# Performance work log

Measured on AMD Instinct MI355X. Metric: run time of the kernel, lower is better.

## Reference

```python
import jax, jax.numpy as jnp
import numpy as np

DECAY = 0.99
EPS = 1e-05
LOSS_FACTOR = 0.1


def setup_inputs() -> dict:
    key = jax.random.key(0)
    k1, k2, k3, k4 = jax.random.split(key, 4)
    x = jax.random.normal(k1, (64, 256, 32, 32), dtype=jnp.float32)
    centroids = jax.random.normal(k2, (256, 1024), dtype=jnp.float32)
    cluster_size = jax.random.uniform(k3, (1024,), dtype=jnp.float32)
    centroids_avg = jax.random.normal(k4, (256, 1024), dtype=jnp.float32)
    return {"x": x, "centroids": centroids, "cluster_size": cluster_size,
            "centroids_avg": centroids_avg}


def _forward(x, centroids, cluster_size, centroids_avg):
    F, K = centroids.shape
    # torch: x_flat = x.transpose(-1, 1).contiguous().view(-1, n_features)
    xs = jnp.swapaxes(x, 1, -1)              # [B, W, H, C]
    flat_shape = xs.shape
    xf = xs.reshape(-1, F)                   # [N, F]
    dist = ((xf * xf).sum(1, keepdims=True)
            + (centroids * centroids).sum(0, keepdims=True)
            - 2.0 * (xf @ centroids))        # [N, K]
    ind = jnp.argmin(dist, axis=1)           # [N] nearest centroid
    # training-path EMA updates (one-hot matmuls expressed as segment sums)
    counts = jax.ops.segment_sum(jnp.ones(ind.shape, dtype=xf.dtype), ind,
                                 num_segments=K)              # [K]
    centroids_sum = jax.ops.segment_sum(xf, ind, num_segments=K).T  # [F, K]
    new_cs = DECAY * cluster_size + (1.0 - DECAY) * counts
    new_avg = DECAY * centroids_avg + (1.0 - DECAY) * centroids_sum
    n = new_cs.sum()
    cs_norm = (new_cs + EPS) / (n + K * EPS) * n
    new_centroids = new_avg / cs_norm[None, :]               # [F, K]
    # quantize with updated codebook (embedding lookup)
    xq = new_centroids.T[ind].reshape(flat_shape)            # [B, W, H, C]
    xq = jnp.swapaxes(xq, 1, -1)                             # [B, C, H, W]
    xq_st = x + jax.lax.stop_gradient(xq - x)                # straight-through
    return xq_st, xq


def reference(x, centroids, cluster_size, centroids_avg):
    out, _ = _forward(x, centroids, cluster_size, centroids_avg)
    return out
```

## Files before the change

### kernel.cpp

```cpp
#include <hip/hip_runtime.h>


#define DECAY 0.99f
#define EPSF 1e-5f
#define DELTA 0.05f

typedef _Float16 f16x8 __attribute__((ext_vector_type(8)));
typedef float f32x4 __attribute__((ext_vector_type(4)));

static __device__ __forceinline__ unsigned short h_bits(_Float16 h) {
  return __builtin_bit_cast(unsigned short, h);
}
static __device__ __forceinline__ float h_val(unsigned short u) {
  return (float)__builtin_bit_cast(_Float16, u);
}

__global__ void centT_kernel(const float* __restrict__ cent, _Float16* __restrict__ ctp,
                             float* __restrict__ csq, unsigned int* __restrict__ counts,
                             unsigned int* __restrict__ flagcnt) {
  __shared__ float tl[32][33];
  const int bid = blockIdx.x;
  const int f0 = (bid >> 5) * 32, k0 = (bid & 31) * 32;
  const int t = threadIdx.x;
#pragma unroll
  for (int i = 0; i < 4; ++i) {
    int fi = (t >> 5) + i * 8, ki = t & 31;
    tl[fi][ki] = cent[(size_t)(f0 + fi) * 1024 + k0 + ki];
  }
  __syncthreads();
#pragma unroll
  for (int i = 0; i < 4; ++i) {
    int ki = (t >> 5) + i * 8, fi = t & 31;
    int k = k0 + ki, f = f0 + fi;
    _Float16 h = (_Float16)tl[fi][ki];
    size_t idx = (size_t)(k >> 4) * 4096 + (size_t)(f >> 5) * 512 +
                 (size_t)(k & 15) * 32 + (size_t)((f >> 3) & 3) * 8 + (f & 7);
    ctp[idx] = h;
  }
  if (bid < 32) {
    __shared__ float red[8][32];
    const int kk = k0 + (t & 31);
    const int fg = t >> 5;
    float s = 0.f;
    for (int f = fg * 32; f < fg * 32 + 32; ++f) {
      float v = cent[(size_t)f * 1024 + kk];
      s += v * v;
    }
    red[fg][t & 31] = s;
    __syncthreads();
    if (t < 32) {
      float tot = 0.f;
#pragma unroll
      for (int g = 0; g < 8; ++g) tot += red[g][t];
      csq[k0 + t] = tot;
    }
  }
  if (bid == 32) {
    counts[t] = 0u;
    counts[t + 256] = 0u;
    counts[t + 512] = 0u;
    counts[t + 768] = 0u;
    if (t == 0) *flagcnt = 0u;
  }
}

__global__ void transpose_kernel(const float* __restrict__ x, _Float16* __restrict__ xh) {
  __shared__ float tile[64][65];
  int bid = blockIdx.x;
  int pt = bid & 15, ct = (bid >> 4) & 3, b = bid >> 6;
  int c0 = ct * 64, p0 = pt * 64;
  int t = threadIdx.x;
#pragma unroll
  for (int i = 0; i < 4; ++i) {
    int idx = t + i * 256;
    int ci = idx >> 4, pq = idx & 15;
    float4 v = *(const float4*)&x[((size_t)(b * 256 + c0 + ci) << 10) + p0 + pq * 4];
    tile[ci][pq * 4 + 0] = v.x;
    tile[ci][pq * 4 + 1] = v.y;
    tile[ci][pq * 4 + 2] = v.z;
    tile[ci][pq * 4 + 3] = v.w;
  }
  __syncthreads();
#pragma unroll
  for (int i = 0; i < 2; ++i) {
    int idx = t + i * 256;
    int pi = idx >> 3, cg = idx & 7;
    int p = p0 + pi;
    int r = ((p & 31) << 5) | (p >> 5);
    unsigned int wd[4];
#pragma unroll
    for (int j = 0; j < 4; ++j) {
      float v0 = tile[cg * 8 + j * 2][pi];
      float v1 = tile[cg * 8 + j * 2 + 1][pi];
      wd[j] = (unsigned int)h_bits((_Float16)v0) |
              ((unsigned int)h_bits((_Float16)v1) << 16);
    }
    uint4 u = {wd[0], wd[1], wd[2], wd[3]};
    *(uint4*)((unsigned int*)xh + (size_t)((b << 10) + r) * 128 + ct * 32 + cg * 4) = u;
  }
}

__global__ __launch_bounds__(256, 2) void mfma_argmin_kernel(
    const _Float16* __restrict__ xh, const _Float16* __restrict__ ctp,
    const float* __restrict__ csq, int* __restrict__ ind,
    int* __restrict__ flaglist, unsigned int* __restrict__ flagcnt,
    unsigned int* __restrict__ counts) {
  __shared__ _Float16 Ah[64 * 256];
  __shared__ _Float16 Bst[4 * 2 * 4 * 512];
  __shared__ float csql[1024];
  __shared__ float red1[4][64], red2[4][64];
  __shared__ int redk[4][64];
  const int t = threadIdx.x;
  const int lane = t & 63, w = t >> 6;
  const int lr = lane & 15, lg = lane >> 4;
  const int n0 = blockIdx.x * 64;

#pragma unroll
  for (int i = 0; i < 4; ++i) csql[t + i * 256] = csq[t + i * 256];
#pragma unroll
  for (int i = 0; i < 8; ++i) {
    int idx = t + i * 256;
    int row = idx >> 5, c16 = (idx & 31) * 16;
    int sw = c16 ^ ((row & 7) << 4);
    *(f16x8*)((char*)Ah + row * 512 + sw) =
        *(const f16x8*)((const char*)xh + (size_t)(n0 + row) * 512 + c16);
  }
  __syncthreads();

  float b1[4][4], b2v[4][4];
  int bk[4][4];
#pragma unroll
  for (int rt = 0; rt < 4; ++rt)
#pragma unroll
    for (int rg = 0; rg < 4; ++rg) { b1[rt][rg] = 3.4e38f; b2v[rt][rg] = 3.4e38f; bk[rt][rg] = 0; }

  const int swz = (lr & 7) << 4;
  const int boffh = (lr * 4 + lg) * 8;
  const size_t lgo = (size_t)lane * 16;
  _Float16* bw = &Bst[w * 4096];

#define DMA4(CHB, KS, P)                                                              \
  do {                                                                                \
    const char* g_ = (const char*)ctp + (CHB) + (size_t)(KS) * 1024 + lgo;            \
    _Float16* l_ = bw + (P) * 2048;                                                   \
    __builtin_amdgcn_global_load_lds(                                                 \
        (const __attribute__((address_space(1))) unsigned int*)(g_),                  \
        (__attribute__((address_space(3))) unsigned int*)(l_), 16, 0, 0);             \
    __builtin_amdgcn_global_load_lds(                                                 \
        (const __attribute__((address_space(1))) unsigned int*)(g_ + 8192),           \
        (__attribute__((address_space(3))) unsigned int*)(l_ + 512), 16, 0, 0);       \
    __builtin_amdgcn_global_load_lds(                                                 \
        (const __attribute__((address_space(1))) unsigned int*)(g_ + 16384),          \
        (__attribute__((address_space(3))) unsigned int*)(l_ + 1024), 16, 0, 0);      \
    __builtin_amdgcn_global_load_lds(                                                 \
        (const __attribute__((address_space(1))) unsigned int*)(g_ + 24576),          \
        (__attribute__((address_space(3))) unsigned int*)(l_ + 1536), 16, 0, 0);      \
  } while (0)

#define KSHALF(KS, P, WN)                                                             \
  do {                                                                                \
    asm volatile("s_waitcnt vmcnt(" WN ")" ::: "memory");                             \
    __builtin_amdgcn_sched_barrier(0);                                                \
    const _Float16* bp_ = bw + (P) * 2048 + boffh;                                    \
    f16x8 q0 = *(const f16x8*)(bp_);                                                  \
    f16x8 q1 = *(const f16x8*)(bp_ + 512);                                            \
    f16x8 q2 = *(const f16x8*)(bp_ + 1024);                                           \
    f16x8 q3 = *(const f16x8*)(bp_ + 1536);                                           \
    const char* ap_ = (const char*)Ah + lr * 512 + (((KS) * 64 + lg * 16) ^ swz);     \
    f16x8 p0 = *(const f16x8*)(ap_);                                                  \
    f16x8 p1 = *(const f16x8*)(ap_ + 8192);                                           \
    f16x8 p2 = *(const f16x8*)(ap_ + 16384);                                          \
    f16x8 p3 = *(const f16x8*)(ap_ + 24576);                                          \
    acc[0][0] = __builtin_amdgcn_mfma_f32_16x16x32_f16(p0, q0, acc[0][0], 0, 0, 0);   \
    acc[0][1] = __builtin_amdgcn_mfma_f32_16x16x32_f16(p1, q0, acc[0][1], 0, 0, 0);   \
    acc[0][2] = __builtin_amdgcn_mfma_f32_16x16x32_f16(p2, q0, acc[0][2], 0, 0, 0);   \
    acc[0][3] = __builtin_amdgcn_mfma_f32_16x16x32_f16(p3, q0, acc[0][3], 0, 0, 0);   \
    acc[1][0] = __builtin_amdgcn_mfma_f32_16x16x32_f16(p0, q1, acc[1][0], 0, 0, 0);   \
    acc[1][1] = __builtin_amdgcn_mfma_f32_16x16x32_f16(p1, q1, acc[1][1], 0, 0, 0);   \
    acc[1][2] = __builtin_amdgcn_mfma_f32_16x16x32_f16(p2, q1, acc[1][2], 0, 0, 0);   \
    acc[1][3] = __builtin_amdgcn_mfma_f32_16x16x32_f16(p3, q1, acc[1][3], 0, 0, 0);   \
    acc[2][0] = __builtin_amdgcn_mfma_f32_16x16x32_f16(p0, q2, acc[2][0], 0, 0, 0);   \
    acc[2][1] = __builtin_amdgcn_mfma_f32_16x16x32_f16(p1, q2, acc[2][1], 0, 0, 0);   \
    acc[2][2] = __builtin_amdgcn_mfma_f32_16x16x32_f16(p2, q2, acc[2][2], 0, 0, 0);   \
    acc[2][3] = __builtin_amdgcn_mfma_f32_16x16x32_f16(p3, q2, acc[2][3], 0, 0, 0);   \
    acc[3][0] = __builtin_amdgcn_mfma_f32_16x16x32_f16(p0, q3, acc[3][0], 0, 0, 0);   \
    acc[3][1] = __builtin_amdgcn_mfma_f32_16x16x32_f16(p1, q3, acc[3][1], 0, 0, 0);   \
    acc[3][2] = __builtin_amdgcn_mfma_f32_16x16x32_f16(p2, q3, acc[3][2], 0, 0, 0);   \
    acc[3][3] = __builtin_amdgcn_mfma_f32_16x16x32_f16(p3, q3, acc[3][3], 0, 0, 0);   \
  } while (0)

  size_t chb = (size_t)w * 131072;
  DMA4(chb, 0, 0);
  DMA4(chb, 1, 1);
#pragma unroll 1
  for (int ch = 0; ch < 4; ++ch) {
    const int ccb = w * 256 + ch * 64;
    f32x4 acc[4][4];
#pragma unroll
    for (int ct = 0; ct < 4; ++ct)
#pragma unroll
      for (int rt = 0; rt < 4; ++rt) acc[ct][rt] = (f32x4){0.f, 0.f, 0.f, 0.f};

    KSHALF(0, 0, "4");  DMA4(chb, 2, 0);
    KSHALF(1, 1, "4");  DMA4(chb, 3, 1);
    KSHALF(2, 0, "4");  DMA4(chb, 4, 0);
    KSHALF(3, 1, "4");  DMA4(chb, 5, 1);
    KSHALF(4, 0, "4");  DMA4(chb, 6, 0);
    KSHALF(5, 1, "4");  DMA4(chb, 7, 1);
    KSHALF(6, 0, "4");
    if (ch < 3) {
      DMA4(chb + 32768, 0, 0);
      KSHALF(7, 1, "4");
      DMA4(chb + 32768, 1, 1);
    } else {
      KSHALF(7, 1, "0");
    }

#pragma unroll
    for (int ct = 0; ct < 4; ++ct) {
      const int col = ccb + ct * 16 + lr;
      const float cq = csql[col];
#pragma unroll
      for (int rt = 0; rt < 4; ++rt)
#pragma unroll
        for (int rg = 0; rg < 4; ++rg) {
          float d = cq - 2.f * acc[ct][rt][rg];
          if (d < b1[rt][rg]) {
            b2v[rt][rg] = b1[rt][rg];
            b1[rt][rg] = d;
            bk[rt][rg] = col;
          } else if (d < b2v[rt][rg]) {
            b2v[rt][rg] = d;
          }
        }
    }
    chb += 32768;
  }
#undef DMA4
#undef KSHALF

#pragma unroll
  for (int rt = 0; rt < 4; ++rt)
#pragma unroll
    for (int rg = 0; rg < 4; ++rg) {
      float v1 = b1[rt][rg], v2 = b2v[rt][rg];
      int kk = bk[rt][rg];
#pragma unroll
      for (int off = 8; off >= 1; off >>= 1) {
        float o1 = __shfl_xor(v1, off);
        int ok = __shfl_xor(kk, off);
        float o2 = __shfl_xor(v2, off);
        float nb2 = fminf(fmaxf(v1, o1), fminf(v2, o2));
        if (o1 < v1 || (o1 == v1 && ok < kk)) { v1 = o1; kk = ok; }
        v2 = nb2;
      }
      if (lr == 0) {
        int row = rt * 16 + lg * 4 + rg;
        red1[w][row] = v1;
        redk[w][row] = kk;
        red2[w][row] = v2;
      }
    }
  __syncthreads();
  if (t < 64) {
    float v1 = red1[0][t], v2 = red2[0][t];
    int kk = redk[0][t];
#pragma unroll
    for (int wi = 1; wi < 4; ++wi) {
      float o1 = red1[wi][t], o2 = red2[wi][t];
      int ok = redk[wi][t];
      float nb2 = fminf(fmaxf(v1, o1), fminf(v2, o2));
      if (o1 < v1 || (o1 == v1 && ok < kk)) { v1 = o1; kk = ok; }
      v2 = nb2;
    }
    ind[n0 + t] = kk;
    atomicAdd(&counts[kk], 1u);
    if (v2 - v1 < DELTA) {
      unsigned int p = atomicAdd(flagcnt, 1u);
      flaglist[p] = n0 + t;
    }
  }
}

__global__ __launch_bounds__(256) void fixup_kernel(
    const float* __restrict__ x, const float* __restrict__ cent,
    const float* __restrict__ csq, const int* __restrict__ flaglist,
    const unsigned int* __restrict__ flagcnt, int* __restrict__ ind,
    unsigned int* __restrict__ counts) {
  const int t = threadIdx.x;
  const int nf = (int)*flagcnt;
  __shared__ float xrow[4][256];
  __shared__ int rows[4];
  __shared__ float rv[256];
  __shared__ int rk[256];
  for (int base = blockIdx.x * 4; base < nf; base += gridDim.x * 4) {
    const int cnt = min(4, nf - base);
    __syncthreads();
    if (t < 4) rows[t] = flaglist[base + (t < cnt ? t : 0)];
    __syncthreads();
#pragma unroll
    for (int j = 0; j < 4; ++j) {
      int row = rows[j];
      int b = row >> 10, r = row & 1023, wq = r >> 5, h = r & 31;
      xrow[j][t] = x[((size_t)(b * 256 + t) << 10) + h * 32 + wq];
    }
    __syncthreads();
    float a[4][4];
#pragma unroll
    for (int j = 0; j < 4; ++j)
#pragma unroll
      for (int q = 0; q < 4; ++q) a[j][q] = 0.f;
#pragma unroll 4
    for (int f = 0; f < 256; ++f) {
      const float* cr = cent + (size_t)f * 1024 + t;
      float c0 = cr[0], c1 = cr[256], c2 = cr[512], c3 = cr[768];
#pragma unroll
      for (int j = 0; j < 4; ++j) {
        float xv = xrow[j][f];
        a[j][0] += xv * c0;
        a[j][1] += xv * c1;
        a[j][2] += xv * c2;
        a[j][3] += xv * c3;
      }
    }
    for (int j = 0; j < cnt; ++j) {
      float bd = csq[t] - 2.f * a[j][0];
      int bkk = t;
      float d1 = csq[t + 256] - 2.f * a[j][1];
      if (d1 < bd) { bd = d1; bkk = t + 256; }
      float d2 = csq[t + 512] - 2.f * a[j][2];
      if (d2 < bd) { bd = d2; bkk = t + 512; }
      float d3 = csq[t + 768] - 2.f * a[j][3];
      if (d3 < bd) { bd = d3; bkk = t + 768; }
      rv[t] = bd;
      rk[t] = bkk;
      __syncthreads();
      for (int off = 128; off >= 1; off >>= 1) {
        if (t < off) {
          float ov = rv[t + off];
          int ok = rk[t + off];
          if (ov < rv[t] || (ov == rv[t] && ok < rk[t])) { rv[t] = ov; rk[t] = ok; }
        }
        __syncthreads();
      }
      if (t == 0) {
        int newk = rk[0], row = rows[j], oldk = ind[row];
        if (newk != oldk) {
          ind[row] = newk;
          atomicAdd(&counts[oldk], 0xFFFFFFFFu);
          atomicAdd(&counts[newk], 1u);
        }
      }
      __syncthreads();
    }
  }
}

__global__ __launch_bounds__(64) void csnorm_scan_kernel(
    const float* __restrict__ cs, const unsigned int* __restrict__ counts,
    float* __restrict__ icn, unsigned int* __restrict__ offsets,
    unsigned int* __restrict__ cursor) {
  const int t = threadIdx.x;
  unsigned int cl[16];
  float csl[16];
  unsigned int s = 0;
  float css = 0.f;
#pragma unroll
  for (int j = 0; j < 16; ++j) {
    cl[j] = counts[t * 16 + j];
    s += cl[j];
    csl[j] = cs[t * 16 + j];
    css += csl[j];
  }
  unsigned int incl = s;
#pragma unroll
  for (int off = 1; off < 64; off <<= 1) {
    unsigned int v = __shfl_up(incl, off);
    if (t >= off) incl += v;
  }
  unsigned int run = incl - s;
  float tot = css;
#pragma unroll
  for (int off = 32; off >= 1; off >>= 1) tot += __shfl_xor(tot, off);
  const float n = DECAY * tot + (1.f - DECAY) * 65536.f;
#pragma unroll
  for (int j = 0; j < 16; ++j) {
    int k = t * 16 + j;
    offsets[k] = run;
    cursor[k] = run;
    float ncs = DECAY * csl[j] + (1.f - DECAY) * (float)cl[j];
    float csn = (ncs + EPSF) / (n + 1024.f * EPSF) * n;
    icn[k] = 1.f / csn;
    run += cl[j];
  }
  if (t == 63) offsets[1024] = run;
}

__global__ void scatter_kernel(const int* __restrict__ ind, unsigned int* __restrict__ cursor,
                               int* __restrict__ rowlist, float4* __restrict__ sums4) {
  int n = blockIdx.x * 256 + threadIdx.x;
  sums4[n] = (float4){0.f, 0.f, 0.f, 0.f};
  int k = ind[n];
  unsigned int pos = atomicAdd(&cursor[k], 1u);
  rowlist[pos] = n;
}

__global__ __launch_bounds__(256) void sumflush_kernel(
    const _Float16* __restrict__ xh, const int* __restrict__ rowlist,
    const int* __restrict__ ind, float* __restrict__ sums) {
  __shared__ int rl[64];
  __shared__ int kl[64];
  const int t = threadIdx.x;
  const int sub = t >> 6, lane = t & 63;
  const int p0 = blockIdx.x * 64;
  if (t < 64) {
    int r = rowlist[p0 + t];
    rl[t] = r;
    kl[t] = ind[r];
  }
  __syncthreads();
  float a0 = 0.f, a1 = 0.f, a2 = 0.f, a3 = 0.f;
  int curk = kl[sub * 16];
#pragma unroll
  for (int i = 0; i < 16; ++i) {
    int p = sub * 16 + i;
    int k = kl[p];
    if (k != curk) {
      float* dst = &sums[(size_t)curk * 256 + lane * 4];
      atomicAdd(&dst[0], a0);
      atomicAdd(&dst[1], a1);
      atomicAdd(&dst[2], a2);
      atomicAdd(&dst[3], a3);
      a0 = a1 = a2 = a3 = 0.f;
      curk = k;
    }
    int r = rl[p];
    uint2 vh = *(const uint2*)&((const unsigned int*)xh)[(size_t)r * 128 + lane * 2];
    a0 += h_val((unsigned short)(vh.x & 0xFFFF));
    a1 += h_val((unsigned short)(vh.x >> 16));
    a2 += h_val((unsigned short)(vh.y & 0xFFFF));
    a3 += h_val((unsigned short)(vh.y >> 16));
  }
  float* dst = &sums[(size_t)curk * 256 + lane * 4];
  atomicAdd(&dst[0], a0);
  atomicAdd(&dst[1], a1);
  atomicAdd(&dst[2], a2);
  atomicAdd(&dst[3], a3);
}

__global__ __launch_bounds__(256) void newcentT_kernel(
    const float* __restrict__ sums, const float* __restrict__ avg,
    const float* __restrict__ icn, float* __restrict__ nc) {
  __shared__ float tl[32][33];
  const int t = threadIdx.x;
  const int k0 = (blockIdx.x & 31) * 32, f0 = (blockIdx.x >> 5) * 32;
#pragma unroll
  for (int i = 0; i < 4; ++i) {
    int ki = (t >> 5) + i * 8, fi = t & 31;
    tl[ki][fi] = sums[(size_t)(k0 + ki) * 256 + f0 + fi];
  }
  __syncthreads();
#pragma unroll
  for (int i = 0; i < 4; ++i) {
    int fi = (t >> 5) + i * 8, ki = t & 31;
    size_t idx = (size_t)(f0 + fi) * 1024 + k0 + ki;
    nc[idx] = (DECAY * avg[idx] + (1.f - DECAY) * tl[ki][fi]) * icn[k0 + ki];
  }
}

__global__ void gather_kernel(const float* __restrict__ nc, const int* __restrict__ ind,
                              float* __restrict__ out) {
  __shared__ int ip[1024];
  int b = blockIdx.x >> 3;
  int cg = (blockIdx.x & 7) * 32;
  int t = threadIdx.x;
#pragma unroll
  for (int j = 0; j < 4; ++j) {
    int p = t + j * 256;
    int r = ((p & 31) << 5) | (p >> 5);
    ip[p] = ind[(b << 10) + r];
  }
  __syncthreads();
  const int p0 = t * 4;
  const int i0 = ip[p0], i1 = ip[p0 + 1], i2 = ip[p0 + 2], i3 = ip[p0 + 3];
  for (int c = cg; c < cg + 32; ++c) {
    const float* row = nc + (size_t)c * 1024;
    float4 v = {row[i0], row[i1], row[i2], row[i3]};
    *(float4*)&out[((size_t)(b * 256 + c) << 10) + p0] = v;
  }
}

extern "C" void kernel_launch(void* const* d_in, const int* in_sizes, int n_in,
                              void* d_out, int out_size, void* d_ws, size_t ws_size,
                              hipStream_t stream) {
  const float* x = (const float*)d_in[0];
  const float* cent = (const float*)d_in[1];
  const float* cs = (const float*)d_in[2];
  const float* avg = (const float*)d_in[3];
  float* out = (float*)d_out;

  char* ws = (char*)d_ws;
  _Float16* xh = (_Float16*)ws;
  _Float16* ctp = (_Float16*)(ws + 33554432);
  float* nc = (float*)(ws + 33554432);
  unsigned int* counts = (unsigned int*)(ws + 34603008);
  unsigned int* flagcnt = (unsigned int*)(ws + 34607104);
  float* csqv = (float*)(ws + 34611200);
  float* icn = (float*)(ws + 34615296);
  unsigned int* offsets = (unsigned int*)(ws + 34619392);
  unsigned int* cursor = (unsigned int*)(ws + 34627584);
  int* ind = (int*)(ws + 34631680);
  int* flaglist = (int*)(ws + 34893824);
  int* rowlist = (int*)(ws + 34893824);
  float* sums = (float*)(ws + 35155968);

  centT_kernel<<<256, 256, 0, stream>>>(cent, ctp, csqv, counts, flagcnt);
  transpose_kernel<<<4096, 256, 0, stream>>>(x, xh);
  mfma_argmin_kernel<<<1024, 256, 0, stream>>>(xh, ctp, csqv, ind, flaglist, flagcnt, counts);
  fixup_kernel<<<256, 256, 0, stream>>>(x, cent, csqv, flaglist, flagcnt, ind, counts);
  csnorm_scan_kernel<<<1, 64, 0, stream>>>(cs, counts, icn, offsets, cursor);
  scatter_kernel<<<256, 256, 0, stream>>>(ind, cursor, rowlist, (float4*)sums);
  sumflush_kernel<<<1024, 256, 0, stream>>>(xh, rowlist, ind, sums);
  newcentT_kernel<<<256, 256, 0, stream>>>(sums, avg, icn, nc);
  gather_kernel<<<512, 256, 0, stream>>>(nc, ind, out);
}
```

Measured before the change: 264.5 us.

## Merge transpose and codebook prep kernels; use fixed-point integer atomics for sums

Measured after the change: 278.8 us, median of 2. 1.05x slower.

```diff
diff --git a/kernel.cpp b/kernel.cpp
--- a/kernel.cpp
+++ b/kernel.cpp
@@ -4,6 +4,7 @@
 #define DECAY 0.99f
 #define EPSF 1e-5f
 #define DELTA 0.05f
+#define FIXSCALE 16777216.f
 
 typedef _Float16 f16x8 __attribute__((ext_vector_type(8)));
 typedef float f32x4 __attribute__((ext_vector_type(4)));
@@ -15,88 +16,90 @@
   return (float)__builtin_bit_cast(_Float16, u);
 }
 
-__global__ void centT_kernel(const float* __restrict__ cent, _Float16* __restrict__ ctp,
-                             float* __restrict__ csq, unsigned int* __restrict__ counts,
-                             unsigned int* __restrict__ flagcnt) {
-  __shared__ float tl[32][33];
+__global__ void transpose_centT_kernel(
+    const float* __restrict__ x, _Float16* __restrict__ xh,
+    const float* __restrict__ cent, _Float16* __restrict__ ctp,
+    float* __restrict__ csq, unsigned int* __restrict__ counts,
+    unsigned int* __restrict__ flagcnt) {
+  __shared__ float smem[64 * 65];
   const int bid = blockIdx.x;
-  const int f0 = (bid >> 5) * 32, k0 = (bid & 31) * 32;
   const int t = threadIdx.x;
-#pragma unroll
-  for (int i = 0; i < 4; ++i) {
-    int fi = (t >> 5) + i * 8, ki = t & 31;
-    tl[fi][ki] = cent[(size_t)(f0 + fi) * 1024 + k0 + ki];
-  }
-  __syncthreads();
-#pragma unroll
-  for (int i = 0; i < 4; ++i) {
-    int ki = (t >> 5) + i * 8, fi = t & 31;
-    int k = k0 + ki, f = f0 + fi;
-    _Float16 h = (_Float16)tl[fi][ki];
-    size_t idx = (size_t)(k >> 4) * 4096 + (size_t)(f >> 5) * 512 +
-                 (size_t)(k & 15) * 32 + (size_t)((f >> 3) & 3) * 8 + (f & 7);
-    ctp[idx] = h;
-  }
-  if (bid < 32) {
-    __shared__ float red[8][32];
-    const int kk = k0 + (t & 31);
-    const int fg = t >> 5;
-    float s = 0.f;
-    for (int f = fg * 32; f < fg * 32 + 32; ++f) {
-      float v = cent[(size_t)f * 1024 + kk];
-      s += v * v;
-    }
-    red[fg][t & 31] = s;
+  if (bid < 4096) {
+    float(*tile)[65] = (float(*)[65])smem;
+    int pt = bid & 15, ct = (bid >> 4) & 3, b = bid >> 6;
+    int c0 = ct * 64, p0 = pt * 64;
+#pragma unroll
+    for (int i = 0; i < 4; ++i) {
+      int idx = t + i * 256;
+      int ci = idx >> 4, pq = idx & 15;
+      float4 v = *(const float4*)&x[((size_t)(b * 256 + c0 + ci) << 10) + p0 + pq * 4];
+      tile[ci][pq * 4 + 0] = v.x;
+      tile[ci][pq * 4 + 1] = v.y;
+      tile[ci][pq * 4 + 2] = v.z;
+      tile[ci][pq * 4 + 3] = v.w;
+    }
     __syncthreads();
-    if (t < 32) {
-      float tot = 0.f;
-#pragma unroll
-      for (int g = 0; g < 8; ++g) tot += red[g][t];
-      csq[k0 + t] = tot;
-    }
-  }
-  if (bid == 32) {
+#pragma unroll
+    for (int i = 0; i < 2; ++i) {
+      int idx = t + i * 256;
+      int pi = idx >> 3, cg = idx & 7;
+      int p = p0 + pi;
+      int r = ((p & 31) << 5) | (p >> 5);
+      unsigned int wd[4];
+#pragma unroll
+      for (int j = 0; j < 4; ++j) {
+        float v0 = tile[cg * 8 + j * 2][pi];
+        float v1 = tile[cg * 8 + j * 2 + 1][pi];
+        wd[j] = (unsigned int)h_bits((_Float16)v0) |
+                ((unsigned int)h_bits((_Float16)v1) << 16);
+      }
+      uint4 u = {wd[0], wd[1], wd[2], wd[3]};
+      *(uint4*)((unsigned int*)xh + (size_t)((b << 10) + r) * 128 + ct * 32 + cg * 4) = u;
+    }
+  } else if (bid < 4352) {
+    const int cid = bid - 4096;
+    const int f0 = (cid >> 5) * 32, k0 = (cid & 31) * 32;
+    float(*tl)[33] = (float(*)[33])smem;
+#pragma unroll
+    for (int i = 0; i < 4; ++i) {
+      int fi = (t >> 5) + i * 8, ki = t & 31;
+      tl[fi][ki] = cent[(size_t)(f0 + fi) * 1024 + k0 + ki];
+    }
+    __syncthreads();
+#pragma unroll
+    for (int i = 0; i < 4; ++i) {
+      int ki = (t >> 5) + i * 8, fi = t & 31;
+      int k = k0 + ki, f = f0 + fi;
+      _Float16 h = (_Float16)tl[fi][ki];
+      size_t idx = (size_t)(k >> 4) * 4096 + (size_t)(f >> 5) * 512 +
+                   (size_t)(k & 15) * 32 + (size_t)((f >> 3) & 3) * 8 + (f & 7);
+      ctp[idx] = h;
+    }
+    if (cid < 32) {
+      float* red = smem + 64 * 33;
+      const int kk = k0 + (t & 31);
+      const int fg = t >> 5;
+      float s = 0.f;
+      for (int f = fg * 32; f < fg * 32 + 32; ++f) {
+        float v = cent[(size_t)f * 1024 + kk];
+        s += v * v;
+      }
+      __syncthreads();
+      red[fg * 32 + (t & 31)] = s;
+      __syncthreads();
+      if (t < 32) {
+        float tot = 0.f;
+#pragma unroll
+        for (int g = 0; g < 8; ++g) tot += red[g * 32 + t];
+        csq[k0 + t] = tot;
+      }
+    }
+  } else {
     counts[t] = 0u;
     counts[t + 256] = 0u;
     counts[t + 512] = 0u;
     counts[t + 768] = 0u;
     if (t == 0) *flagcnt = 0u;
-  }
-}
-
-__global__ void transpose_kernel(const float* __restrict__ x, _Float16* __restrict__ xh) {
-  __shared__ float tile[64][65];
-  int bid = blockIdx.x;
-  int pt = bid & 15, ct = (bid >> 4) & 3, b = bid >> 6;
-  int c0 = ct * 64, p0 = pt * 64;
-  int t = threadIdx.x;
-#pragma unroll
-  for (int i = 0; i < 4; ++i) {
-    int idx = t + i * 256;
-    int ci = idx >> 4, pq = idx & 15;
-    float4 v = *(const float4*)&x[((size_t)(b * 256 + c0 + ci) << 10) + p0 + pq * 4];
-    tile[ci][pq * 4 + 0] = v.x;
-    tile[ci][pq * 4 + 1] = v.y;
-    tile[ci][pq * 4 + 2] = v.z;
-    tile[ci][pq * 4 + 3] = v.w;
-  }
-  __syncthreads();
-#pragma unroll
-  for (int i = 0; i < 2; ++i) {
-    int idx = t + i * 256;
-    int pi = idx >> 3, cg = idx & 7;
-    int p = p0 + pi;
-    int r = ((p & 31) << 5) | (p >> 5);
-    unsigned int wd[4];
-#pragma unroll
-    for (int j = 0; j < 4; ++j) {
-      float v0 = tile[cg * 8 + j * 2][pi];
-      float v1 = tile[cg * 8 + j * 2 + 1][pi];
-      wd[j] = (unsigned int)h_bits((_Float16)v0) |
-              ((unsigned int)h_bits((_Float16)v1) << 16);
-    }
-    uint4 u = {wd[0], wd[1], wd[2], wd[3]};
-    *(uint4*)((unsigned int*)xh + (size_t)((b << 10) + r) * 128 + ct * 32 + cg * 4) = u;
   }
 }
 
@@ -397,9 +400,11 @@
 }
 
 __global__ void scatter_kernel(const int* __restrict__ ind, unsigned int* __restrict__ cursor,
-                               int* __restrict__ rowlist, float4* __restrict__ sums4) {
+                               int* __restrict__ rowlist, uint4* __restrict__ isums4) {
   int n = blockIdx.x * 256 + threadIdx.x;
-  sums4[n] = (float4){0.f, 0.f, 0.f, 0.f};
+  uint4 z = {0u, 0u, 0u, 0u};
+  isums4[n * 2] = z;
+  isums4[n * 2 + 1] = z;
   int k = ind[n];
   unsigned int pos = atomicAdd(&cursor[k], 1u);
   rowlist[pos] = n;
@@ -407,7 +412,7 @@
 
 __global__ __launch_bounds__(256) void sumflush_kernel(
     const _Float16* __restrict__ xh, const int* __restrict__ rowlist,
-    const int* __restrict__ ind, float* __restrict__ sums) {
+    const int* __restrict__ ind, unsigned long long* __restrict__ isums) {
   __shared__ int rl[64];
   __shared__ int kl[64];
   const int t = threadIdx.x;
@@ -419,37 +424,37 @@
     kl[t] = ind[r];
   }
   __syncthreads();
-  float a0 = 0.f, a1 = 0.f, a2 = 0.f, a3 = 0.f;
+  long long a0 = 0, a1 = 0, a2 = 0, a3 = 0;
   int curk = kl[sub * 16];
 #pragma unroll
   for (int i = 0; i < 16; ++i) {
     int p = sub * 16 + i;
     int k = kl[p];
     if (k != curk) {
-      float* dst = &sums[(size_t)curk * 256 + lane * 4];
-      atomicAdd(&dst[0], a0);
-      atomicAdd(&dst[1], a1);
-      atomicAdd(&dst[2], a2);
-      atomicAdd(&dst[3], a3);
-      a0 = a1 = a2 = a3 = 0.f;
+      unsigned long long* dst = &isums[(size_t)curk * 256 + lane * 4];
+      atomicAdd(&dst[0], (unsigned long long)a0);
+      atomicAdd(&dst[1], (unsigned long long)a1);
+      atomicAdd(&dst[2], (unsigned long long)a2);
+      atomicAdd(&dst[3], (unsigned long long)a3);
+      a0 = a1 = a2 = a3 = 0;
       curk = k;
     }
     int r = rl[p];
     uint2 vh = *(const uint2*)&((const unsigned int*)xh)[(size_t)r * 128 + lane * 2];
-    a0 += h_val((unsigned short)(vh.x & 0xFFFF));
-    a1 += h_val((unsigned short)(vh.x >> 16));
-    a2 += h_val((unsigned short)(vh.y & 0xFFFF));
-    a3 += h_val((unsigned short)(vh.y >> 16));
-  }
-  float* dst = &sums[(size_t)curk * 256 + lane * 4];
-  atomicAdd(&dst[0], a0);
-  atomicAdd(&dst[1], a1);
-  atomicAdd(&dst[2], a2);
-  atomicAdd(&dst[3], a3);
+    a0 += (long long)llrintf(h_val((unsigned short)(vh.x & 0xFFFF)) * FIXSCALE);
+    a1 += (long long)llrintf(h_val((unsigned short)(vh.x >> 16)) * FIXSCALE);
+    a2 += (long long)llrintf(h_val((unsigned short)(vh.y & 0xFFFF)) * FIXSCALE);
+    a3 += (long long)llrintf(h_val((unsigned short)(vh.y >> 16)) * FIXSCALE);
+  }
+  unsigned long long* dst = &isums[(size_t)curk * 256 + lane * 4];
+  atomicAdd(&dst[0], (unsigned long long)a0);
+  atomicAdd(&dst[1], (unsigned long long)a1);
+  atomicAdd(&dst[2], (unsigned long long)a2);
+  atomicAdd(&dst[3], (unsigned long long)a3);
 }
 
 __global__ __launch_bounds__(256) void newcentT_kernel(
-    const float* __restrict__ sums, const float* __restrict__ avg,
+    const unsigned long long* __restrict__ isums, const float* __restrict__ avg,
     const float* __restrict__ icn, float* __restrict__ nc) {
   __shared__ float tl[32][33];
   const int t = threadIdx.x;
@@ -457,7 +462,8 @@
 #pragma unroll
   for (int i = 0; i < 4; ++i) {
     int ki = (t >> 5) + i * 8, fi = t & 31;
-    tl[ki][fi] = sums[(size_t)(k0 + ki) * 256 + f0 + fi];
+    long long iv = (long long)isums[(size_t)(k0 + ki) * 256 + f0 + fi];
+    tl[ki][fi] = (float)((double)iv * (1.0 / 16777216.0));
   }
   __syncthreads();
 #pragma unroll
@@ -512,15 +518,14 @@
   int* ind = (int*)(ws + 34631680);
   int* flaglist = (int*)(ws + 34893824);
   int* rowlist = (int*)(ws + 34893824);
-  float* sums = (float*)(ws + 35155968);
-
-  centT_kernel<<<256, 256, 0, stream>>>(cent, ctp, csqv, counts, flagcnt);
-  transpose_kernel<<<4096, 256, 0, stream>>>(x, xh);
+  unsigned long long* isums = (unsigned long long*)(ws + 35155968);
+
+  transpose_centT_kernel<<<4353, 256, 0, stream>>>(x, xh, cent, ctp, csqv, counts, flagcnt);
   mfma_argmin_kernel<<<1024, 256, 0, stream>>>(xh, ctp, csqv, ind, flaglist, flagcnt, counts);
   fixup_kernel<<<256, 256, 0, stream>>>(x, cent, csqv, flaglist, flagcnt, ind, counts);
   csnorm_scan_kernel<<<1, 64, 0, stream>>>(cs, counts, icn, offsets, cursor);
-  scatter_kernel<<<256, 256, 0, stream>>>(ind, cursor, rowlist, (float4*)sums);
-  sumflush_kernel<<<1024, 256, 0, stream>>>(xh, rowlist, ind, sums);
-  newcentT_kernel<<<256, 256, 0, stream>>>(sums, avg, icn, nc);
+  scatter_kernel<<<256, 256, 0, stream>>>(ind, cursor, rowlist, (uint4*)isums);
+  sumflush_kernel<<<1024, 256, 0, stream>>>(xh, rowlist, ind, isums);
+  newcentT_kernel<<<256, 256, 0, stream>>>(isums, avg, icn, nc);
   gather_kernel<<<512, 256, 0, stream>>>(nc, ind, out);
 }
```
